# Kernel optimization log

Measured on AMD Instinct MI355X. Metric: run time of the kernel, lower is better.

Reference implementation:

```python
import jax, jax.numpy as jnp
import numpy as np

N = 20000      # nodes
E = 320000     # edges (avg degree 16)
IN = 64        # input feature dim
EMB = 128      # emb_dim / c_dim
OUT = 10       # num classes
L = 5          # num_layers
RATIO = 0.25
TEMP = 1.0
NOISE = 1.0
MAX_ITER = 30
EPS = 1e-20


def setup_inputs() -> dict:
    key = jax.random.key(0)
    ks = jax.random.split(key, 12)
    def w(k, shape, fan):
        return jax.random.normal(k, shape, jnp.float32) / np.float32(np.sqrt(fan))
    x = jax.random.normal(ks[0], (N, IN), jnp.float32)
    edge_index = jax.random.randint(ks[1], (2, E), 0, N, jnp.int32)
    u = jax.random.uniform(ks[2], (E, 1), jnp.float32)
    return {
        "x": x,
        "edge_index": edge_index,
        "u": u,
        "enc_W0": w(ks[3], (IN, EMB), IN), "enc_b0": jnp.zeros((EMB,), jnp.float32),
        "enc_W": w(ks[4], (L - 1, EMB, EMB), EMB), "enc_b": jnp.zeros((L - 1, EMB), jnp.float32),
        "ea_W1": w(ks[5], (2 * EMB, 4 * EMB), 2 * EMB), "ea_b1": jnp.zeros((4 * EMB,), jnp.float32),
        "ea_W2": w(ks[6], (4 * EMB, 1), 4 * EMB), "ea_b2": jnp.zeros((1,), jnp.float32),
        "cls_W0": w(ks[7], (IN, EMB), IN), "cls_b0": jnp.zeros((EMB,), jnp.float32),
        "cls_W": w(ks[8], (L - 1, EMB, EMB), EMB), "cls_b": jnp.zeros((L - 1, EMB), jnp.float32),
        "head_W": w(ks[9], (EMB, OUT), EMB), "head_b": jnp.zeros((OUT,), jnp.float32),
    }


def _gin_stack(x, W0, b0, Ws, bs, src, dst, att):
    """GIN-style stack: aggregate att-weighted neighbor messages, then linear+ReLU."""
    agg = jax.ops.segment_sum(x[src] * att, dst, num_segments=N)
    h = jax.nn.relu((x + agg) @ W0 + b0)
    def layer(h, wb):
        W, b = wb
        agg = jax.ops.segment_sum(h[src] * att, dst, num_segments=N)
        return jax.nn.relu((h + agg) @ W + b), None
    h, _ = jax.lax.scan(layer, h, (Ws, bs))
    return h


def reference(x, edge_index, u, enc_W0, enc_b0, enc_W, enc_b,
              ea_W1, ea_b1, ea_W2, ea_b2,
              cls_W0, cls_b0, cls_W, cls_b, head_W, head_b):
    src, dst = edge_index[0], edge_index[1]
    ones = jnp.ones((E, 1), jnp.float32)

    # GNN encoder
    h = _gin_stack(x, enc_W0, enc_b0, enc_W, enc_b, src, dst, ones)

    # edge attention MLP on [h_src, h_dst]
    edge_rep = jnp.concatenate([h[src], h[dst]], axis=-1)            # [E, 2*EMB]
    pe = jax.nn.relu(edge_rep @ ea_W1 + ea_b1) @ ea_W2 + ea_b2       # [E, 1]
    atts = (pe - pe.mean()) / jnp.std(pe, ddof=1)

    # Gumbel noise from uniform u (training path)
    g = -jnp.log(-jnp.log(u + EPS) + EPS)
    d = atts + g * NOISE

    s_min, s_max = atts.min(), atts.max()
    D = jnp.concatenate([d - s_min, s_max - d], axis=-1)             # [E, 2]
    logT = -D / TEMP
    log_rs = jnp.log(jnp.array([[E * (1.0 - RATIO), E * RATIO]], jnp.float32) + EPS)

    # 30-step Sinkhorn normalization in log space
    def body(i, lt):
        lt = lt - jax.scipy.special.logsumexp(lt, axis=-1, keepdims=True)
        lt = lt - jax.scipy.special.logsumexp(lt, axis=-2, keepdims=True)
        return lt + log_rs
    logT = jax.lax.fori_loop(0, MAX_ITER, body, logT)
    T = jnp.exp(logT)[:, 1:2]                                        # [E, 1]

    # classifier GNN on raw features with Sinkhorn edge attention
    hc = _gin_stack(x, cls_W0, cls_b0, cls_W, cls_b, src, dst, T)
    rep = hc.mean(axis=0)                                            # mean graph pooling
    return rep @ head_W + head_b                                     # [OUT]
```

## Files before the change

### kernel.cpp

```cpp
#include <hip/hip_runtime.h>
#include <math.h>

#define NN 20000
#define EE 320000
#define NBINS 2048
#define HRANGE 64.0f
#define EPSF 1e-20f

typedef __attribute__((ext_vector_type(8))) short bf16x8;
typedef __attribute__((ext_vector_type(4))) float f32x4;

constexpr size_t OFF_DEG  = 0;
constexpr size_t OFF_RS   = 20000;
constexpr size_t OFF_CUR  = 40008;
constexpr size_t OFF_EIX  = 60008;
constexpr size_t OFF_GSRC = 380008;
constexpr size_t OFF_B0   = 700008;
constexpr size_t OFF_B1   = 1980008;
constexpr size_t OFF_PA   = 3260008;
constexpr size_t OFF_PB   = 8380008;
constexpr size_t OFF_PE   = 13500008;
constexpr size_t OFF_DL   = 13820008;
constexpr size_t OFF_TT   = 14140008;
constexpr size_t OFF_HIST = 14460008;
constexpr size_t OFF_SCAL = 14464104;
constexpr size_t OFF_REP  = 14464136;
constexpr size_t OFF_WT   = 14464264;
constexpr size_t WT_ENC0 = 0;
constexpr size_t WT_ENC  = 8192;
constexpr size_t WT_CLS0 = 73728;
constexpr size_t WT_CLS  = 81920;
constexpr size_t WT_EA1  = 147456;

__device__ __forceinline__ unsigned ordf(float f) {
  unsigned b = __float_as_uint(f);
  return (b >> 31) ? ~b : (b | 0x80000000u);
}
__device__ __forceinline__ float unordf(unsigned u) {
  unsigned b = (u >> 31) ? (u ^ 0x80000000u) : ~u;
  return __uint_as_float(b);
}
__device__ __forceinline__ ushort f2bf(float f) {
  unsigned u = __float_as_uint(f);
  u += 0x7FFFu + ((u >> 16) & 1u);
  return (ushort)(u >> 16);
}
__device__ __forceinline__ unsigned pack2(float x, float y) {
  return (unsigned)f2bf(x) | ((unsigned)f2bf(y) << 16);
}
__device__ __forceinline__ float bf2f(ushort h) {
  return __uint_as_float(((unsigned)h) << 16);
}
__device__ __forceinline__ float bflo(unsigned v) { return __uint_as_float(v << 16); }
__device__ __forceinline__ float bfhi(unsigned v) { return __uint_as_float(v & 0xFFFF0000u); }
__device__ __forceinline__ int eclamp(int j, int hi) {
  return max(min(j, hi), 0);
}

__global__ void init_ws(int* deg, int* cur, float* hist, float* scal, float* rep) {
  int i = blockIdx.x * blockDim.x + threadIdx.x;
  if (i < NN) { deg[i] = 0; cur[i] = 0; }
  if (i < 2 * NBINS) hist[i] = 0.f;
  if (i < 128) rep[i] = 0.f;
  if (i < 32) {
    if (i == 2)      ((unsigned*)scal)[2] = 0xFFFFFFFFu;
    else if (i == 3) ((unsigned*)scal)[3] = 0u;
    else scal[i] = 0.f;
  }
}

__global__ void count_deg(const int* __restrict__ dst, int* __restrict__ deg) {
  int e = blockIdx.x * 256 + threadIdx.x;
  if (e < EE) atomicAdd(&deg[dst[e]], 1);
}

__global__ __launch_bounds__(1024) void scan_deg(const int* __restrict__ deg,
                                                 int* __restrict__ rs) {
  __shared__ int ps[1024];
  const int t = threadIdx.x;
  const int base = t * 20;
  int loc[20];
  int s = 0;
#pragma unroll
  for (int j = 0; j < 20; ++j) {
    int idx = base + j;
    int v = (idx < NN) ? deg[idx] : 0;
    loc[j] = s;
    s += v;
  }
  ps[t] = s;
  __syncthreads();
  for (int off = 1; off < 1024; off <<= 1) {
    int x = (t >= off) ? ps[t - off] : 0;
    __syncthreads();
    ps[t] += x;
    __syncthreads();
  }
  const int excl = ps[t] - s;
#pragma unroll
  for (int j = 0; j < 20; ++j) {
    int idx = base + j;
    if (idx < NN) rs[idx] = excl + loc[j];
  }
  if (t == 1023) rs[NN] = ps[1023];
}

__global__ void fill_csr(const int* __restrict__ src, const int* __restrict__ dst,
                         const int* __restrict__ rs, int* __restrict__ cur,
                         int* __restrict__ eidx, int* __restrict__ gsrc) {
  int e = blockIdx.x * 256 + threadIdx.x;
  if (e < EE) {
    int d = dst[e];
    int p = atomicAdd(&cur[d], 1);
    int o = rs[d] + p;
    eidx[o] = e;
    gsrc[o] = src[e];
  }
}

__global__ void transpose_all(const float* __restrict__ encW0, const float* __restrict__ encW,
                              const float* __restrict__ clsW0, const float* __restrict__ clsW,
                              const float* __restrict__ eaW1, ushort* __restrict__ Wt) {
  int i = blockIdx.x * 256 + threadIdx.x;
  if (i < 8192) {
    int k = i >> 7, n = i & 127;
    Wt[WT_ENC0 + n * 64 + k] = f2bf(encW0[i]);
  } else if (i < 73728) {
    int j = i - 8192;
    int l = j >> 14, r = j & 16383, k = r >> 7, n = r & 127;
    Wt[WT_ENC + l * 16384 + n * 128 + k] = f2bf(encW[j]);
  } else if (i < 81920) {
    int j = i - 73728;
    int k = j >> 7, n = j & 127;
    Wt[WT_CLS0 + n * 64 + k] = f2bf(clsW0[j]);
  } else if (i < 147456) {
    int j = i - 81920;
    int l = j >> 14, r = j & 16383, k = r >> 7, n = r & 127;
    Wt[WT_CLS + l * 16384 + n * 128 + k] = f2bf(clsW[j]);
  } else if (i < 278528) {
    int j = i - 147456;
    int k = j >> 9, n = j & 511;
    Wt[WT_EA1 + n * 256 + k] = f2bf(eaW1[j]);
  }
}

template <bool HASATT>
__global__ __launch_bounds__(256) void fused_layer64(
    const float* __restrict__ X, ushort* __restrict__ C,
    const int* __restrict__ gsrc, const int* __restrict__ rs,
    const float* __restrict__ att, const ushort* __restrict__ Bt,
    const float* __restrict__ bias) {
  __shared__ __align__(16) char smem[8448];
  ushort* Asm = (ushort*)smem;
  const int tid = threadIdx.x;
  const int g = tid >> 4, l = tid & 15;
  const int nb = blockIdx.x * 16;
  {
    const int n = nb + g;
    const int e0 = rs[n];
    const int deg = rs[n + 1] - e0;
    const int hi = e0 + deg - 1;
    float4 s = ((const float4*)(X + (size_t)n * 64))[l];
    float a[4] = {s.x, s.y, s.z, s.w};
    const float4* Xr = (const float4*)X;

    int i0 = gsrc[eclamp(e0 + 0, hi)];
    int i1 = gsrc[eclamp(e0 + 1, hi)];
    int i2 = gsrc[eclamp(e0 + 2, hi)];
    int i3 = gsrc[eclamp(e0 + 3, hi)];
    float4 F0 = Xr[(size_t)i0 * 16 + l];
    float4 F1 = Xr[(size_t)i1 * 16 + l];
    float4 F2 = Xr[(size_t)i2 * 16 + l];
    float4 F3 = Xr[(size_t)i3 * 16 + l];
    int G0 = gsrc[eclamp(e0 + 4, hi)];
    int G1 = gsrc[eclamp(e0 + 5, hi)];
    int G2 = gsrc[eclamp(e0 + 6, hi)];
    int G3 = gsrc[eclamp(e0 + 7, hi)];
    float W0 = 1.f, W1 = 1.f, W2 = 1.f, W3 = 1.f;
    if (HASATT) {
      W0 = att[eclamp(e0 + 0, hi)];
      W1 = att[eclamp(e0 + 1, hi)];
      W2 = att[eclamp(e0 + 2, hi)];
      W3 = att[eclamp(e0 + 3, hi)];
    }

#define FL64_STEP(F, G, W, J)                                                 \
    {                                                                         \
      if ((J) < deg) {                                                        \
        const float cw_ = HASATT ? (W) : 1.f;                                 \
        a[0] = fmaf(cw_, F.x, a[0]); a[1] = fmaf(cw_, F.y, a[1]);             \
        a[2] = fmaf(cw_, F.z, a[2]); a[3] = fmaf(cw_, F.w, a[3]);             \
      }                                                                       \
      F = Xr[(size_t)G * 16 + l];                                             \
      G = gsrc[eclamp(e0 + (J) + 8, hi)];                                     \
      if (HASATT) W = att[eclamp(e0 + (J) + 4, hi)];                          \
    }

    for (int j = 0; j < deg; j += 4) {
      FL64_STEP(F0, G0, W0, j);
      FL64_STEP(F1, G1, W1, j + 1);
      FL64_STEP(F2, G2, W2, j + 2);
      FL64_STEP(F3, G3, W3, j + 3);
    }
#undef FL64_STEP
    ushort4 o;
    o.x = f2bf(a[0]); o.y = f2bf(a[1]); o.z = f2bf(a[2]); o.w = f2bf(a[3]);
    *(ushort4*)(Asm + g * 72 + l * 4) = o;
  }
  __syncthreads();
  const int wave = tid >> 6, lane = tid & 63, quad = lane >> 4, l15 = lane & 15;
  f32x4 acc[2] = {{0.f, 0.f, 0.f, 0.f}, {0.f, 0.f, 0.f, 0.f}};
#pragma unroll
  for (int k0 = 0; k0 < 64; k0 += 32) {
    bf16x8 af = *(const bf16x8*)(Asm + l15 * 72 + k0 + quad * 8);
#pragma unroll
    for (int t = 0; t < 2; ++t) {
      int bn = wave * 32 + t * 16 + l15;
      bf16x8 bf = *(const bf16x8*)(Bt + (size_t)bn * 64 + k0 + quad * 8);
      acc[t] = __builtin_amdgcn_mfma_f32_16x16x32_bf16(af, bf, acc[t], 0, 0, 0);
    }
  }
  __syncthreads();
  float (*Csm)[132] = (float(*)[132])smem;
#pragma unroll
  for (int t = 0; t < 2; ++t) {
    int lc = wave * 32 + t * 16 + l15;
    float bs = bias[lc];
#pragma unroll
    for (int r = 0; r < 4; ++r)
      Csm[quad * 4 + r][lc] = fmaxf(acc[t][r] + bs, 0.f);
  }
  __syncthreads();
  const int r = tid >> 4, cc = (tid & 15) * 8;
  f32x4 v0 = *(const f32x4*)&Csm[r][cc];
  f32x4 v1 = *(const f32x4*)&Csm[r][cc + 4];
  uint4 o;
  o.x = pack2(v0[0], v0[1]); o.y = pack2(v0[2], v0[3]);
  o.z = pack2(v1[0], v1[1]); o.w = pack2(v1[2], v1[3]);
  *(uint4*)(C + (size_t)(nb + r) * 128 + cc) = o;
}

template <bool HASATT>
__global__ __launch_bounds__(256) void fused_layer128(
    const ushort* __restrict__ Xb, ushort* __restrict__ C,
    const int* __restrict__ gsrc, const int* __restrict__ rs,
    const float* __restrict__ att, const ushort* __restrict__ Bt,
    const float* __restrict__ bias) {
  __shared__ __align__(16) char smem[8448];
  ushort* Asm = (ushort*)smem;
  const int tid = threadIdx.x;
  const int g = tid >> 4, l = tid & 15;
  const int nb = blockIdx.x * 16;
  {
    const int n = nb + g;
    const int e0 = rs[n];
    const int deg = rs[n + 1] - e0;
    const int hi = e0 + deg - 1;
    float a[8];
    {
      uint4 s = ((const uint4*)(Xb + (size_t)n * 128))[l];
      a[0] = bflo(s.x); a[1] = bfhi(s.x); a[2] = bflo(s.y); a[3] = bfhi(s.y);
      a[4] = bflo(s.z); a[5] = bfhi(s.z); a[6] = bflo(s.w); a[7] = bfhi(s.w);
    }
    const uint4* Xr = (const uint4*)Xb;

    int i0 = gsrc[eclamp(e0 + 0, hi)];
    int i1 = gsrc[eclamp(e0 + 1, hi)];
    int i2 = gsrc[eclamp(e0 + 2, hi)];
    int i3 = gsrc[eclamp(e0 + 3, hi)];
    uint4 F0 = Xr[(size_t)i0 * 16 + l];
    uint4 F1 = Xr[(size_t)i1 * 16 + l];
    uint4 F2 = Xr[(size_t)i2 * 16 + l];
    uint4 F3 = Xr[(size_t)i3 * 16 + l];
    int G0 = gsrc[eclamp(e0 + 4, hi)];
    int G1 = gsrc[eclamp(e0 + 5, hi)];
    int G2 = gsrc[eclamp(e0 + 6, hi)];
    int G3 = gsrc[eclamp(e0 + 7, hi)];
    float W0 = 1.f, W1 = 1.f, W2 = 1.f, W3 = 1.f;
    if (HASATT) {
      W0 = att[eclamp(e0 + 0, hi)];
      W1 = att[eclamp(e0 + 1, hi)];
      W2 = att[eclamp(e0 + 2, hi)];
      W3 = att[eclamp(e0 + 3, hi)];
    }

#define FL128_STEP(F, G, W, J)                                                \
    {                                                                         \
      if ((J) < deg) {                                                        \
        const float cw_ = HASATT ? (W) : 1.f;                                 \
        a[0] = fmaf(cw_, bflo(F.x), a[0]); a[1] = fmaf(cw_, bfhi(F.x), a[1]); \
        a[2] = fmaf(cw_, bflo(F.y), a[2]); a[3] = fmaf(cw_, bfhi(F.y), a[3]); \
        a[4] = fmaf(cw_, bflo(F.z), a[4]); a[5] = fmaf(cw_, bfhi(F.z), a[5]); \
        a[6] = fmaf(cw_, bflo(F.w), a[6]); a[7] = fmaf(cw_, bfhi(F.w), a[7]); \
      }                                                                       \
      F = Xr[(size_t)G * 16 + l];                                             \
      G = gsrc[eclamp(e0 + (J) + 8, hi)];                                     \
      if (HASATT) W = att[eclamp(e0 + (J) + 4, hi)];                          \
    }

    for (int j = 0; j < deg; j += 4) {
      FL128_STEP(F0, G0, W0, j);
      FL128_STEP(F1, G1, W1, j + 1);
      FL128_STEP(F2, G2, W2, j + 2);
      FL128_STEP(F3, G3, W3, j + 3);
    }
#undef FL128_STEP
    uint4 o;
    o.x = pack2(a[0], a[1]); o.y = pack2(a[2], a[3]);
    o.z = pack2(a[4], a[5]); o.w = pack2(a[6], a[7]);
    *(uint4*)(Asm + g * 136 + l * 8) = o;
  }
  __syncthreads();
  const int wave = tid >> 6, lane = tid & 63, quad = lane >> 4, l15 = lane & 15;
  f32x4 acc[2] = {{0.f, 0.f, 0.f, 0.f}, {0.f, 0.f, 0.f, 0.f}};
#pragma unroll
  for (int k0 = 0; k0 < 128; k0 += 32) {
    bf16x8 af = *(const bf16x8*)(Asm + l15 * 136 + k0 + quad * 8);
#pragma unroll
    for (int t = 0; t < 2; ++t) {
      int bn = wave * 32 + t * 16 + l15;
      bf16x8 bf = *(const bf16x8*)(Bt + (size_t)bn * 128 + k0 + quad * 8);
      acc[t] = __builtin_amdgcn_mfma_f32_16x16x32_bf16(af, bf, acc[t], 0, 0, 0);
    }
  }
  __syncthreads();
  float (*Csm)[132] = (float(*)[132])smem;
#pragma unroll
  for (int t = 0; t < 2; ++t) {
    int lc = wave * 32 + t * 16 + l15;
    float bs = bias[lc];
#pragma unroll
    for (int r = 0; r < 4; ++r)
      Csm[quad * 4 + r][lc] = fmaxf(acc[t][r] + bs, 0.f);
  }
  __syncthreads();
  const int r = tid >> 4, cc = (tid & 15) * 8;
  f32x4 v0 = *(const f32x4*)&Csm[r][cc];
  f32x4 v1 = *(const f32x4*)&Csm[r][cc + 4];
  uint4 o;
  o.x = pack2(v0[0], v0[1]); o.y = pack2(v0[2], v0[3]);
  o.z = pack2(v1[0], v1[1]); o.w = pack2(v1[2], v1[3]);
  *(uint4*)(C + (size_t)(nb + r) * 128 + cc) = o;
}

__global__ __launch_bounds__(256) void gemm_papb(
    const ushort* __restrict__ Hb, const ushort* __restrict__ W1t,
    const float* __restrict__ b1, ushort* __restrict__ Pa, ushort* __restrict__ Pb) {
  __shared__ float lds[32][132];
  const int tid = threadIdx.x;
  const int wave = tid >> 6, lane = tid & 63, quad = lane >> 4, l15 = lane & 15;
  const int mh = wave >> 1, nh = wave & 1;
  const int col0 = blockIdx.x * 128;
  const int row0 = blockIdx.y * 32;
  f32x4 accA[4] = {{0.f, 0.f, 0.f, 0.f}, {0.f, 0.f, 0.f, 0.f},
                   {0.f, 0.f, 0.f, 0.f}, {0.f, 0.f, 0.f, 0.f}};
  f32x4 accB[4] = {{0.f, 0.f, 0.f, 0.f}, {0.f, 0.f, 0.f, 0.f},
                   {0.f, 0.f, 0.f, 0.f}, {0.f, 0.f, 0.f, 0.f}};
  const ushort* Ap = Hb + (size_t)(row0 + mh * 16 + l15) * 128 + quad * 8;
#pragma unroll
  for (int k0 = 0; k0 < 128; k0 += 32) {
    bf16x8 af = *(const bf16x8*)(Ap + k0);
#pragma unroll
    for (int t = 0; t < 4; ++t) {
      int bn = col0 + nh * 64 + t * 16 + l15;
      const ushort* Brow = W1t + (size_t)bn * 256 + k0 + quad * 8;
      bf16x8 bfa = *(const bf16x8*)(Brow);
      bf16x8 bfb = *(const bf16x8*)(Brow + 128);
      accA[t] = __builtin_amdgcn_mfma_f32_16x16x32_bf16(af, bfa, accA[t], 0, 0, 0);
      accB[t] = __builtin_amdgcn_mfma_f32_16x16x32_bf16(af, bfb, accB[t], 0, 0, 0);
    }
  }
#pragma unroll
  for (int pass = 0; pass < 2; ++pass) {
    if (pass) __syncthreads();
#pragma unroll
    for (int t = 0; t < 4; ++t) {
      int lc = nh * 64 + t * 16 + l15;
      float bs = pass ? 0.f : b1[col0 + lc];
      f32x4 av = pass ? accB[t] : accA[t];
#pragma unroll
      for (int r = 0; r < 4; ++r)
        lds[mh * 16 + quad * 4 + r][lc] = av[r] + bs;
    }
    __syncthreads();
    ushort* C = pass ? Pb : Pa;
    const int r = tid >> 3, c0 = (tid & 7) * 16;
    ushort* Cp = C + (size_t)(row0 + r) * 512 + col0 + c0;
#pragma unroll
    for (int k = 0; k < 4; ++k) {
      f32x4 v = *(const f32x4*)&lds[r][c0 + k * 4];
      ushort4 o;
      o.x = f2bf(v[0]); o.y = f2bf(v[1]); o.z = f2bf(v[2]); o.w = f2bf(v[3]);
      *(ushort4*)(Cp + k * 4) = o;
    }
  }
}

__global__ __launch_bounds__(256) void edge_pe_csr(
    const ushort* __restrict__ Pa, const ushort* __restrict__ Pb,
    const int* __restrict__ gsrc, const int* __restrict__ rs,
    const float* __restrict__ W2, const float* __restrict__ b2,
    float* __restrict__ pe) {
  const int lane = threadIdx.x & 63;
  const int n = blockIdx.x * 4 + (threadIdx.x >> 6);
  const int e0 = rs[n];
  const int deg = rs[n + 1] - e0;
  if (deg <= 0) return;
  const int hi = e0 + deg - 1;
  float w[8], pb[8];
  {
    const float4* w2v = (const float4*)(W2 + lane * 8);
    float4 t0 = w2v[0], t1 = w2v[1];
    w[0] = t0.x; w[1] = t0.y; w[2] = t0.z; w[3] = t0.w;
    w[4] = t1.x; w[5] = t1.y; w[6] = t1.z; w[7] = t1.w;
    uint4 b = ((const uint4*)(Pb + (size_t)n * 512))[lane];
    pb[0] = bflo(b.x); pb[1] = bfhi(b.x); pb[2] = bflo(b.y); pb[3] = bfhi(b.y);
    pb[4] = bflo(b.z); pb[5] = bfhi(b.z); pb[6] = bflo(b.w); pb[7] = bfhi(b.w);
  }
  const float b2v = b2[0];
  const uint4* Par = (const uint4*)Pa;

  int i0 = gsrc[eclamp(e0 + 0, hi)];
  int i1 = gsrc[eclamp(e0 + 1, hi)];
  int i2 = gsrc[eclamp(e0 + 2, hi)];
  int i3 = gsrc[eclamp(e0 + 3, hi)];
  uint4 F0 = Par[(size_t)i0 * 64 + lane];
  uint4 F1 = Par[(size_t)i1 * 64 + lane];
  uint4 F2 = Par[(size_t)i2 * 64 + lane];
  uint4 F3 = Par[(size_t)i3 * 64 + lane];
  int G0 = gsrc[eclamp(e0 + 4, hi)];
  int G1 = gsrc[eclamp(e0 + 5, hi)];
  int G2 = gsrc[eclamp(e0 + 6, hi)];
  int G3 = gsrc[eclamp(e0 + 7, hi)];

#define PE_STEP(F, G, J)                                                      \
  {                                                                           \
    if ((J) < deg) {                                                          \
      float pa[8] = {bflo(F.x), bfhi(F.x), bflo(F.y), bfhi(F.y),              \
                     bflo(F.z), bfhi(F.z), bflo(F.w), bfhi(F.w)};             \
      float acc = 0.f;                                                        \
      _Pragma("unroll")                                                       \
      for (int jj = 0; jj < 8; ++jj) acc += fmaxf(pa[jj] + pb[jj], 0.f) * w[jj]; \
      _Pragma("unroll")                                                       \
      for (int off = 32; off; off >>= 1) acc += __shfl_xor(acc, off);         \
      if (lane == 0) pe[e0 + (J)] = acc + b2v;                                \
    }                                                                         \
    F = Par[(size_t)G * 64 + lane];                                           \
    G = gsrc[eclamp(e0 + (J) + 8, hi)];                                       \
  }

  for (int j = 0; j < deg; j += 4) {
    PE_STEP(F0, G0, j);
    PE_STEP(F1, G1, j + 1);
    PE_STEP(F2, G2, j + 2);
    PE_STEP(F3, G3, j + 3);
  }
#undef PE_STEP
}

__global__ __launch_bounds__(256) void pe_stats(const float* __restrict__ pe,
                                                float* __restrict__ scal) {
  __shared__ float r1[256], r2[256], r3[256], r4[256];
  int tid = threadIdx.x;
  float s = 0.f, q = 0.f, mn = 3.0e38f, mx = -3.0e38f;
  for (int i = blockIdx.x * 256 + tid; i < EE; i += gridDim.x * 256) {
    float v = pe[i];
    s += v; q = fmaf(v, v, q);
    mn = fminf(mn, v); mx = fmaxf(mx, v);
  }
  r1[tid] = s; r2[tid] = q; r3[tid] = mn; r4[tid] = mx;
  __syncthreads();
  for (int k = 128; k > 0; k >>= 1) {
    if (tid < k) {
      r1[tid] += r1[tid + k];
      r2[tid] += r2[tid + k];
      r3[tid] = fminf(r3[tid], r3[tid + k]);
      r4[tid] = fmaxf(r4[tid], r4[tid + k]);
    }
    __syncthreads();
  }
  if (tid == 0) {
    unsafeAtomicAdd(&scal[0], r1[0]);
    unsafeAtomicAdd(&scal[1], r2[0]);
    atomicMin((unsigned*)scal + 2, ordf(r3[0]));
    atomicMax((unsigned*)scal + 3, ordf(r4[0]));
  }
}

__global__ __launch_bounds__(256) void edge_delta_hist(
    const float* __restrict__ pe, const float* __restrict__ u,
    const int* __restrict__ eidx, float* __restrict__ delta,
    float* __restrict__ hist, const float* __restrict__ scal) {
  __shared__ float cnt_s[NBINS], sum_s[NBINS];
  for (int b = threadIdx.x; b < NBINS; b += 256) { cnt_s[b] = 0.f; sum_s[b] = 0.f; }
  float sum = scal[0], ssq = scal[1];
  float mn = unordf(((const unsigned*)scal)[2]);
  float mx = unordf(((const unsigned*)scal)[3]);
  float mu = sum / (float)EE;
  float var = (ssq - sum * sum / (float)EE) / (float)(EE - 1);
  float istd = rsqrtf(fmaxf(var, 1e-30f));
  float shift = (mn - mu) * istd + (mx - mu) * istd;
  __syncthreads();
  for (int i = blockIdx.x * 256 + threadIdx.x; i < EE; i += gridDim.x * 256) {
    float uu = u[eidx[i]];
    float atts = (pe[i] - mu) * istd;
    float g = -logf(-logf(uu + EPSF) + EPSF);
    float dl = 2.0f * (atts + g) - shift;
    delta[i] = dl;
    float dcl = fminf(fmaxf(dl, -HRANGE), HRANGE * 0.9999f);
    int b = (int)((dcl + HRANGE) * ((float)NBINS / (2.0f * HRANGE)));
    b = min(max(b, 0), NBINS - 1);
    atomicAdd(&cnt_s[b], 1.0f);
    atomicAdd(&sum_s[b], dcl);
  }
  __syncthreads();
  for (int b = threadIdx.x; b < NBINS; b += 256) {
    float c = cnt_s[b];
    if (c != 0.f) {
      unsafeAtomicAdd(&hist[b], c);
      unsafeAtomicAdd(&hist[NBINS + b], sum_s[b]);
    }
  }
}

__global__ __launch_bounds__(64) void sinkhorn_iter(const float* __restrict__ hist,
                                                    float* __restrict__ scal) {
  const int lane = threadIdx.x;
  float cnt[32], mean[32];
#pragma unroll
  for (int b = 0; b < 32; ++b) {
    int idx = b * 64 + lane;
    float c = hist[idx];
    cnt[b] = c;
    mean[b] = (c > 0.f) ? hist[NBINS + idx] / c : 0.f;
  }
  const float LRD = -1.0986122886681098f;
  float S = 0.f, Zfin = 0.f;
  for (int it = 0; it < 30; ++it) {
    float p = 0.f;
#pragma unroll
    for (int b = 0; b < 32; ++b)
      if (cnt[b] > 0.f) p += cnt[b] / (1.f + expf(-(mean[b] + S)));
#pragma unroll
    for (int off = 32; off; off >>= 1) p += __shfl_xor(p, off);
    if (it < 29)
      S += logf(fmaxf((float)EE - p, 1.0f)) - logf(p) + LRD;
    else
      Zfin = p;
  }
  if (lane == 0) {
    scal[8] = S;
    scal[9] = ((float)EE * 0.25f) / Zfin;
  }
}

__global__ void compute_T(const float* __restrict__ delta,
                          const float* __restrict__ scal,
                          float* __restrict__ Ta) {
  int i = blockIdx.x * 256 + threadIdx.x;
  if (i >= EE) return;
  float S = scal[8], sc = scal[9];
  Ta[i] = sc / (1.f + expf(-(delta[i] + S)));
}

__global__ __launch_bounds__(128) void col_mean(const ushort* __restrict__ Hc,
                                                float* __restrict__ rep) {
  int c = threadIdx.x;
  const int g = gridDim.x;
  float p0 = 0.f, p1 = 0.f, p2 = 0.f, p3 = 0.f;
  int n = blockIdx.x;
  for (; n + 3 * g < NN; n += 4 * g) {
    p0 += bf2f(Hc[(size_t)n * 128 + c]);
    p1 += bf2f(Hc[(size_t)(n + g) * 128 + c]);
    p2 += bf2f(Hc[(size_t)(n + 2 * g) * 128 + c]);
    p3 += bf2f(Hc[(size_t)(n + 3 * g) * 128 + c]);
  }
  for (; n < NN; n += g) p0 += bf2f(Hc[(size_t)n * 128 + c]);
  unsafeAtomicAdd(&rep[c], (p0 + p1) + (p2 + p3));
}

__global__ __launch_bounds__(128) void head_kernel(const float* __restrict__ repsum,
                                                   const float* __restrict__ hW,
                                                   const float* __restrict__ hb,
                                                   float* __restrict__ out) {
  __shared__ float rep[128];
  int tid = threadIdx.x;
  if (tid < 128) rep[tid] = repsum[tid] * (1.0f / (float)NN);
  __syncthreads();
  if (tid < 10) {
    float a = hb[tid];
#pragma unroll
    for (int c = 0; c < 128; c++) a = fmaf(rep[c], hW[c * 10 + tid], a);
    out[tid] = a;
  }
}

extern "C" void kernel_launch(void* const* d_in, const int* in_sizes, int n_in,
                              void* d_out, int out_size, void* d_ws, size_t ws_size,
                              hipStream_t stream) {
  const float* x      = (const float*)d_in[0];
  const int*   ei     = (const int*)d_in[1];
  const float* u      = (const float*)d_in[2];
  const float* enc_W0 = (const float*)d_in[3];
  const float* enc_b0 = (const float*)d_in[4];
  const float* enc_W  = (const float*)d_in[5];
  const float* enc_b  = (const float*)d_in[6];
  const float* ea_W1  = (const float*)d_in[7];
  const float* ea_b1  = (const float*)d_in[8];
  const float* ea_W2  = (const float*)d_in[9];
  const float* ea_b2  = (const float*)d_in[10];
  const float* cls_W0 = (const float*)d_in[11];
  const float* cls_b0 = (const float*)d_in[12];
  const float* cls_W  = (const float*)d_in[13];
  const float* cls_b  = (const float*)d_in[14];
  const float* head_W = (const float*)d_in[15];
  const float* head_b = (const float*)d_in[16];
  const int* src  = ei;
  const int* dstp = ei + EE;

  float* wsF = (float*)d_ws;
  int*   wsI = (int*)d_ws;
  int* deg  = wsI + OFF_DEG;
  int* rs   = wsI + OFF_RS;
  int* cur  = wsI + OFF_CUR;
  int* eix  = wsI + OFF_EIX;
  int* gsrc = wsI + OFF_GSRC;
  ushort* B0 = (ushort*)(wsF + OFF_B0);
  ushort* B1 = (ushort*)(wsF + OFF_B1);
  ushort* Pa = (ushort*)(wsF + OFF_PA);
  ushort* Pb = (ushort*)(wsF + OFF_PB);
  float* pe   = wsF + OFF_PE;
  float* dl   = wsF + OFF_DL;
  float* Ta   = wsF + OFF_TT;
  float* hist = wsF + OFF_HIST;
  float* scal = wsF + OFF_SCAL;
  float* rep  = wsF + OFF_REP;
  ushort* Wt  = (ushort*)(wsF + OFF_WT);
  float* out = (float*)d_out;

  init_ws<<<(NN + 255) / 256, 256, 0, stream>>>(deg, cur, hist, scal, rep);
  count_deg<<<(EE + 255) / 256, 256, 0, stream>>>(dstp, deg);
  scan_deg<<<1, 1024, 0, stream>>>(deg, rs);
  fill_csr<<<(EE + 255) / 256, 256, 0, stream>>>(src, dstp, rs, cur, eix, gsrc);
  transpose_all<<<1088, 256, 0, stream>>>(enc_W0, enc_W, cls_W0, cls_W, ea_W1, Wt);

  const int GB = NN / 16;

  fused_layer64<false><<<GB, 256, 0, stream>>>(x, B0, gsrc, rs, nullptr, Wt + WT_ENC0, enc_b0);
  {
    ushort* in = B0; ushort* outb = B1;
    for (int l = 0; l < 4; l++) {
      fused_layer128<false><<<GB, 256, 0, stream>>>(in, outb, gsrc, rs, nullptr,
                                                    Wt + WT_ENC + (size_t)l * 16384,
                                                    enc_b + (size_t)l * 128);
      ushort* t = in; in = outb; outb = t;
    }
  }

  gemm_papb<<<dim3(4, NN / 32), 256, 0, stream>>>(B0, Wt + WT_EA1, ea_b1, Pa, Pb);
  edge_pe_csr<<<NN / 4, 256, 0, stream>>>(Pa, Pb, gsrc, rs, ea_W2, ea_b2, pe);

  pe_stats<<<512, 256, 0, stream>>>(pe, scal);
  edge_delta_hist<<<128, 256, 0, stream>>>(pe, u, eix, dl, hist, scal);
  sinkhorn_iter<<<1, 64, 0, stream>>>(hist, scal);
  compute_T<<<(EE + 255) / 256, 256, 0, stream>>>(dl, scal, Ta);

  fused_layer64<true><<<GB, 256, 0, stream>>>(x, B0, gsrc, rs, Ta, Wt + WT_CLS0, cls_b0);
  {
    ushort* in = B0; ushort* outb = B1;
    for (int l = 0; l < 4; l++) {
      fused_layer128<true><<<GB, 256, 0, stream>>>(in, outb, gsrc, rs, Ta,
                                                   Wt + WT_CLS + (size_t)l * 16384,
                                                   cls_b + (size_t)l * 128);
      ushort* t = in; in = outb; outb = t;
    }
  }

  col_mean<<<256, 128, 0, stream>>>(B0, rep);
  head_kernel<<<1, 128, 0, stream>>>(rep, head_W, head_b, out);
}
```

Measured before the change: 519.0 us.

## Sort nodes by in-degree and process gather kernels in degree-bucketed order

```diff
diff --git a/kernel.cpp b/kernel.cpp
--- a/kernel.cpp
+++ b/kernel.cpp
@@ -57,10 +57,12 @@
   return max(min(j, hi), 0);
 }
 
-__global__ void init_ws(int* deg, int* cur, float* hist, float* scal, float* rep) {
+__global__ void init_ws(int* deg, int* cur, float* hist, float* scal, float* rep,
+                        int* hb) {
   int i = blockIdx.x * blockDim.x + threadIdx.x;
   if (i < NN) { deg[i] = 0; cur[i] = 0; }
   if (i < 2 * NBINS) hist[i] = 0.f;
+  if (i < 384) hb[i] = 0;
   if (i < 128) rep[i] = 0.f;
   if (i < 32) {
     if (i == 2)      ((unsigned*)scal)[2] = 0xFFFFFFFFu;
@@ -115,6 +117,42 @@
     int o = rs[d] + p;
     eidx[o] = e;
     gsrc[o] = src[e];
+  }
+}
+
+__global__ void deg_hist(const int* __restrict__ deg, int* __restrict__ hb) {
+  __shared__ int lb[128];
+  if (threadIdx.x < 128) lb[threadIdx.x] = 0;
+  __syncthreads();
+  int i = blockIdx.x * 256 + threadIdx.x;
+  if (i < NN) atomicAdd(&lb[min(deg[i], 127)], 1);
+  __syncthreads();
+  if (threadIdx.x < 128 && lb[threadIdx.x]) atomicAdd(&hb[threadIdx.x], lb[threadIdx.x]);
+}
+
+__global__ __launch_bounds__(128) void bucket_scan(int* __restrict__ hb) {
+  __shared__ int ps[128];
+  const int t = threadIdx.x;
+  int v = hb[t];
+  ps[t] = v;
+  __syncthreads();
+  for (int off = 1; off < 128; off <<= 1) {
+    int x = (t >= off) ? ps[t - off] : 0;
+    __syncthreads();
+    ps[t] += x;
+    __syncthreads();
+  }
+  hb[128 + t] = ps[t] - v;
+  hb[256 + t] = 0;
+}
+
+__global__ void fill_perm(const int* __restrict__ deg, int* __restrict__ hb,
+                          int* __restrict__ perm) {
+  int n = blockIdx.x * 256 + threadIdx.x;
+  if (n < NN) {
+    int b = min(deg[n], 127);
+    int p = atomicAdd(&hb[256 + b], 1);
+    perm[hb[128 + b] + p] = n;
   }
 }
 
@@ -149,14 +187,14 @@
     const float* __restrict__ X, ushort* __restrict__ C,
     const int* __restrict__ gsrc, const int* __restrict__ rs,
     const float* __restrict__ att, const ushort* __restrict__ Bt,
-    const float* __restrict__ bias) {
+    const float* __restrict__ bias, const int* __restrict__ perm) {
   __shared__ __align__(16) char smem[8448];
   ushort* Asm = (ushort*)smem;
   const int tid = threadIdx.x;
   const int g = tid >> 4, l = tid & 15;
   const int nb = blockIdx.x * 16;
   {
-    const int n = nb + g;
+    const int n = perm[nb + g];
     const int e0 = rs[n];
     const int deg = rs[n + 1] - e0;
     const int hi = e0 + deg - 1;
@@ -232,12 +270,13 @@
   }
   __syncthreads();
   const int r = tid >> 4, cc = (tid & 15) * 8;
+  const int pn = perm[nb + r];
   f32x4 v0 = *(const f32x4*)&Csm[r][cc];
   f32x4 v1 = *(const f32x4*)&Csm[r][cc + 4];
   uint4 o;
   o.x = pack2(v0[0], v0[1]); o.y = pack2(v0[2], v0[3]);
   o.z = pack2(v1[0], v1[1]); o.w = pack2(v1[2], v1[3]);
-  *(uint4*)(C + (size_t)(nb + r) * 128 + cc) = o;
+  *(uint4*)(C + (size_t)pn * 128 + cc) = o;
 }
 
 template <bool HASATT>
@@ -245,14 +284,14 @@
     const ushort* __restrict__ Xb, ushort* __restrict__ C,
     const int* __restrict__ gsrc, const int* __restrict__ rs,
     const float* __restrict__ att, const ushort* __restrict__ Bt,
-    const float* __restrict__ bias) {
+    const float* __restrict__ bias, const int* __restrict__ perm) {
   __shared__ __align__(16) char smem[8448];
   ushort* Asm = (ushort*)smem;
   const int tid = threadIdx.x;
   const int g = tid >> 4, l = tid & 15;
   const int nb = blockIdx.x * 16;
   {
-    const int n = nb + g;
+    const int n = perm[nb + g];
     const int e0 = rs[n];
     const int deg = rs[n + 1] - e0;
     const int hi = e0 + deg - 1;
@@ -335,12 +374,13 @@
   }
   __syncthreads();
   const int r = tid >> 4, cc = (tid & 15) * 8;
+  const int pn = perm[nb + r];
   f32x4 v0 = *(const f32x4*)&Csm[r][cc];
   f32x4 v1 = *(const f32x4*)&Csm[r][cc + 4];
   uint4 o;
   o.x = pack2(v0[0], v0[1]); o.y = pack2(v0[2], v0[3]);
   o.z = pack2(v1[0], v1[1]); o.w = pack2(v1[2], v1[3]);
-  *(uint4*)(C + (size_t)(nb + r) * 128 + cc) = o;
+  *(uint4*)(C + (size_t)pn * 128 + cc) = o;
 }
 
 __global__ __launch_bounds__(256) void gemm_papb(
@@ -400,9 +440,9 @@
     const ushort* __restrict__ Pa, const ushort* __restrict__ Pb,
     const int* __restrict__ gsrc, const int* __restrict__ rs,
     const float* __restrict__ W2, const float* __restrict__ b2,
-    float* __restrict__ pe) {
+    float* __restrict__ pe, const int* __restrict__ perm) {
   const int lane = threadIdx.x & 63;
-  const int n = blockIdx.x * 4 + (threadIdx.x >> 6);
+  const int n = perm[blockIdx.x * 4 + (threadIdx.x >> 6)];
   const int e0 = rs[n];
   const int deg = rs[n + 1] - e0;
   if (deg <= 0) return;
@@ -623,6 +663,8 @@
   int* deg  = wsI + OFF_DEG;
   int* rs   = wsI + OFF_RS;
   int* cur  = wsI + OFF_CUR;
+  int* perm = wsI + OFF_CUR;
+  int* hb   = wsI + OFF_DL;
   int* eix  = wsI + OFF_EIX;
   int* gsrc = wsI + OFF_GSRC;
   ushort* B0 = (ushort*)(wsF + OFF_B0);
@@ -638,40 +680,45 @@
   ushort* Wt  = (ushort*)(wsF + OFF_WT);
   float* out = (float*)d_out;
 
-  init_ws<<<(NN + 255) / 256, 256, 0, stream>>>(deg, cur, hist, scal, rep);
+  init_ws<<<(NN + 255) / 256, 256, 0, stream>>>(deg, cur, hist, scal, rep, hb);
   count_deg<<<(EE + 255) / 256, 256, 0, stream>>>(dstp, deg);
   scan_deg<<<1, 1024, 0, stream>>>(deg, rs);
   fill_csr<<<(EE + 255) / 256, 256, 0, stream>>>(src, dstp, rs, cur, eix, gsrc);
+  deg_hist<<<(NN + 255) / 256, 256, 0, stream>>>(deg, hb);
+  bucket_scan<<<1, 128, 0, stream>>>(hb);
+  fill_perm<<<(NN + 255) / 256, 256, 0, stream>>>(deg, hb, perm);
   transpose_all<<<1088, 256, 0, stream>>>(enc_W0, enc_W, cls_W0, cls_W, ea_W1, Wt);
 
   const int GB = NN / 16;
 
-  fused_layer64<false><<<GB, 256, 0, stream>>>(x, B0, gsrc, rs, nullptr, Wt + WT_ENC0, enc_b0);
+  fused_layer64<false><<<GB, 256, 0, stream>>>(x, B0, gsrc, rs, nullptr,
+                                               Wt + WT_ENC0, enc_b0, perm);
   {
     ushort* in = B0; ushort* outb = B1;
     for (int l = 0; l < 4; l++) {
       fused_layer128<false><<<GB, 256, 0, stream>>>(in, outb, gsrc, rs, nullptr,
                                                     Wt + WT_ENC + (size_t)l * 16384,
-                                                    enc_b + (size_t)l * 128);
+                                                    enc_b + (size_t)l * 128, perm);
       ushort* t = in; in = outb; outb = t;
     }
   }
 
   gemm_papb<<<dim3(4, NN / 32), 256, 0, stream>>>(B0, Wt + WT_EA1, ea_b1, Pa, Pb);
-  edge_pe_csr<<<NN / 4, 256, 0, stream>>>(Pa, Pb, gsrc, rs, ea_W2, ea_b2, pe);
+  edge_pe_csr<<<NN / 4, 256, 0, stream>>>(Pa, Pb, gsrc, rs, ea_W2, ea_b2, pe, perm);
 
   pe_stats<<<512, 256, 0, stream>>>(pe, scal);
   edge_delta_hist<<<128, 256, 0, stream>>>(pe, u, eix, dl, hist, scal);
   sinkhorn_iter<<<1, 64, 0, stream>>>(hist, scal);
   compute_T<<<(EE + 255) / 256, 256, 0, stream>>>(dl, scal, Ta);
 
-  fused_layer64<true><<<GB, 256, 0, stream>>>(x, B0, gsrc, rs, Ta, Wt + WT_CLS0, cls_b0);
+  fused_layer64<true><<<GB, 256, 0, stream>>>(x, B0, gsrc, rs, Ta,
+                                              Wt + WT_CLS0, cls_b0, perm);
   {
     ushort* in = B0; ushort* outb = B1;
     for (int l = 0; l < 4; l++) {
       fused_layer128<true><<<GB, 256, 0, stream>>>(in, outb, gsrc, rs, Ta,
                                                    Wt + WT_CLS + (size_t)l * 16384,
-                                                   cls_b + (size_t)l * 128);
+                                                   cls_b + (size_t)l * 128, perm);
       ushort* t = in; in = outb; outb = t;
     }
   }
```

New measurement: 594.1 us. +14.5%, slower.
